# Performance work log

Measured on AMD Instinct MI355X. Metric: run time of the kernel, lower is better.

Reference implementation:

```python
import jax, jax.numpy as jnp
import numpy as np

HIDDEN = 64
EMBED = 16
N_AGENTS = 1024
TRACK_LEN = 8


def setup_inputs() -> dict:
    key = jax.random.key(0)
    ks = jax.random.split(key, 6)
    s = lambda fan_in: 1.0 / np.sqrt(fan_in)
    return {
        "hidden_state": jax.random.normal(ks[0], (1, N_AGENTS, HIDDEN), jnp.float32),
        "group_track": jax.random.normal(ks[1], (N_AGENTS, TRACK_LEN, 2), jnp.float32),
        "W_e": jax.random.normal(ks[2], (2, EMBED), jnp.float32) * s(2),
        "b_e": jnp.zeros((EMBED,), jnp.float32),
        "W1": jax.random.normal(ks[3], (EMBED + HIDDEN, 2 * HIDDEN), jnp.float32) * s(EMBED + HIDDEN),
        "b1": jnp.zeros((2 * HIDDEN,), jnp.float32),
        "W2": jax.random.normal(ks[4], (2 * HIDDEN, HIDDEN), jnp.float32) * s(2 * HIDDEN),
        "b2": jnp.zeros((HIDDEN,), jnp.float32),
    }


def reference(hidden_state, group_track, W_e, b_e, W1, b1, W2, b2):
    n = group_track.shape[0]
    ends = group_track[:, -1, :]                       # [N, 2] end positions
    # rel[c, j] = end_j - end_c  (relative neighbor end pos per center agent)
    rel = ends[None, :, :] - ends[:, None, :]          # [N, N, 2]
    emb = rel @ W_e + b_e                              # [N, N, E]
    h = jnp.broadcast_to(hidden_state[0][None, :, :], (n, n, hidden_state.shape[-1]))
    x = jnp.concatenate([h, emb], axis=-1)             # [N, N, E+H] (hidden first, as in torch)
    y = jax.nn.relu(x @ W1 + b1)                       # [N, N, 2H]
    z = jax.nn.relu(y @ W2 + b2)                       # [N, N, H]
    pooled = z.max(axis=1)                             # max over neighbors -> [N, H]
    return pooled[None]                                # [1, N, H]
```

## Files before the change

### kernel.cpp

```cpp
#include <hip/hip_runtime.h>


#define N_AG 1024

typedef __attribute__((ext_vector_type(8))) short short8;
typedef __attribute__((ext_vector_type(4))) float floatx4;
typedef __attribute__((ext_vector_type(4))) unsigned int uintx4;

#if defined(__has_builtin)
#if __has_builtin(__builtin_amdgcn_cvt_pk_bf16_f32)
#define HAVE_CVT_PK_BF16 1
typedef __bf16 bf16x2 __attribute__((ext_vector_type(2)));
#endif
#endif

__device__ __forceinline__ unsigned short f2bf(float f) {
  unsigned u = __builtin_bit_cast(unsigned, f);
  u += 0x7FFFu + ((u >> 16) & 1u);
  return (unsigned short)(u >> 16);
}

__device__ __forceinline__ unsigned pack2bf(float y0, float y1) {
#ifdef HAVE_CVT_PK_BF16
  bf16x2 pk = __builtin_amdgcn_cvt_pk_bf16_f32(y0, y1);
  return __builtin_bit_cast(unsigned, pk);
#else
  return (unsigned)f2bf(y0) | ((unsigned)f2bf(y1) << 16);
#endif
}

__global__ __launch_bounds__(128) void prep_all(
    const float* __restrict__ hidden,
    const float* __restrict__ track,
    const float* __restrict__ We,
    const float* __restrict__ be,
    const float* __restrict__ W1,
    const float* __restrict__ b1,
    const float* __restrict__ W2,
    unsigned short* __restrict__ Abf,
    float* __restrict__ M2f,
    unsigned short* __restrict__ W2T)
{
  int j = blockIdx.x;
  int k = threadIdx.x;
  __shared__ float hj[64];
  if (k < 64) hj[k] = hidden[j * 64 + k];
  __syncthreads();
  float e0 = track[j * 16 + 14];
  float e1 = track[j * 16 + 15];
  float m20 = 0.f, m21 = 0.f, cb = b1[k];
#pragma unroll
  for (int t = 0; t < 16; ++t) {
    float w1v = W1[(64 + t) * 128 + k];
    m20 += We[t] * w1v;
    m21 += We[16 + t] * w1v;
    cb  += be[t] * w1v;
  }
  float acc = e0 * m20 + e1 * m21 + cb;
#pragma unroll 16
  for (int t = 0; t < 64; ++t) acc += hj[t] * W1[t * 128 + k];
  Abf[j * 128 + k] = f2bf(acc);

  if (j == 0) {
    M2f[k]       = m20;
    M2f[128 + k] = m21;
  }
  if (j < 32) {
#pragma unroll
    for (int q = 0; q < 2; ++q) {
      int idx = j * 256 + q * 128 + k;
      int n = idx >> 7, c = idx & 127;
      W2T[n * 128 + c] = f2bf(W2[c * 64 + n]);
    }
  }
}

__global__ __launch_bounds__(256) void pool_main(
    const unsigned short* __restrict__ Abf,
    const float* __restrict__ M2f,
    const float* __restrict__ track,
    const unsigned short* __restrict__ W2T,
    const float* __restrict__ b2,
    float* __restrict__ out)
{
  const int i    = blockIdx.x;
  const int lane = threadIdx.x & 63;
  const int wave = threadIdx.x >> 6;
  const int m    = lane & 15;
  const int quad = lane >> 4;

  const float e0 = track[i * 16 + 14];
  const float e1 = track[i * 16 + 15];
  float u[4][8];
#pragma unroll
  for (int kk = 0; kk < 4; ++kk) {
#pragma unroll
    for (int jj = 0; jj < 8; ++jj) {
      int kidx = kk * 32 + quad * 8 + jj;
      u[kk][jj] = e0 * M2f[kidx] + e1 * M2f[128 + kidx];
    }
  }

  short8 bfrag[4][4];
#pragma unroll
  for (int t = 0; t < 4; ++t)
#pragma unroll
    for (int kk = 0; kk < 4; ++kk)
      bfrag[t][kk] = *(const short8*)(W2T + (t * 16 + m) * 128 + kk * 32 + quad * 8);

  floatx4 mx[4];
#pragma unroll
  for (int t = 0; t < 4; ++t) mx[t] = (floatx4){-3e38f, -3e38f, -3e38f, -3e38f};

  for (int jt = wave; jt < 64; jt += 4) {
    const unsigned short* Aptr = Abf + (jt * 16 + m) * 128 + quad * 8;
    uintx4 au[4];
#pragma unroll
    for (int kk = 0; kk < 4; ++kk) {
      uintx4 raw = *(const uintx4*)(Aptr + kk * 32);
#pragma unroll
      for (int p = 0; p < 4; ++p) {
        unsigned w = raw[p];
        float lo = __builtin_bit_cast(float, w << 16);
        float hi = __builtin_bit_cast(float, w & 0xFFFF0000u);
        float y0 = fmaxf(lo - u[kk][2 * p], 0.f);
        float y1 = fmaxf(hi - u[kk][2 * p + 1], 0.f);
        au[kk][p] = pack2bf(y0, y1);
      }
    }
#pragma unroll
    for (int t = 0; t < 4; ++t) {
      floatx4 acc = (floatx4){0.f, 0.f, 0.f, 0.f};
#pragma unroll
      for (int kk = 0; kk < 4; ++kk) {
        short8 af = __builtin_bit_cast(short8, au[kk]);
        acc = __builtin_amdgcn_mfma_f32_16x16x32_bf16(af, bfrag[t][kk], acc, 0, 0, 0);
      }
#pragma unroll
      for (int r = 0; r < 4; ++r) mx[t][r] = fmaxf(mx[t][r], acc[r]);
    }
  }

  float lm[4];
#pragma unroll
  for (int t = 0; t < 4; ++t) {
    lm[t] = fmaxf(fmaxf(mx[t][0], mx[t][1]), fmaxf(mx[t][2], mx[t][3]));
    lm[t] = fmaxf(lm[t], __shfl_xor(lm[t], 16, 64));
    lm[t] = fmaxf(lm[t], __shfl_xor(lm[t], 32, 64));
  }
  __shared__ float red[4][64];
  if (quad == 0) {
#pragma unroll
    for (int t = 0; t < 4; ++t) red[wave][t * 16 + m] = lm[t];
  }
  __syncthreads();
  if (threadIdx.x < 64) {
    int n = threadIdx.x;
    float v = fmaxf(fmaxf(red[0][n], red[1][n]), fmaxf(red[2][n], red[3][n]));
    v += b2[n];
    v = v > 0.f ? v : 0.f;
    out[i * 64 + n] = v;
  }
}

extern "C" void kernel_launch(void* const* d_in, const int* in_sizes, int n_in,
                              void* d_out, int out_size, void* d_ws, size_t ws_size,
                              hipStream_t stream) {
  const float* hidden = (const float*)d_in[0];
  const float* track  = (const float*)d_in[1];
  const float* We     = (const float*)d_in[2];
  const float* be     = (const float*)d_in[3];
  const float* W1     = (const float*)d_in[4];
  const float* b1     = (const float*)d_in[5];
  const float* W2     = (const float*)d_in[6];
  const float* b2     = (const float*)d_in[7];
  float* out = (float*)d_out;

  char* ws = (char*)d_ws;
  unsigned short* Abf = (unsigned short*)ws;
  float*          M2f = (float*)(ws + 262144);
  unsigned short* W2T = (unsigned short*)(ws + 263168);

  prep_all<<<N_AG, 128, 0, stream>>>(hidden, track, We, be, W1, b1, W2, Abf, M2f, W2T);
  pool_main<<<N_AG, 256, 0, stream>>>(Abf, M2f, track, W2T, b2, out);
}
```

Baseline: 113.5 us.

## Prefetch next A tile in pool loop and force hardware bf16 pack

The main pooling loop now issues the global loads for the next neighbor tile before the current tile's ReLU, pack and MFMA work, using register double-buffering to hide load latency. The bf16 pack now always uses inline v_cvt_pk_bf16_f32 assembly instead of the builtin-or-fallback path, so the software rounding sequence cannot be selected. The prep kernel writes the A matrix with nontemporal stores. The prefetch buffer raises register pressure, which could reduce occupancy.

```diff
diff --git a/kernel.cpp b/kernel.cpp
--- a/kernel.cpp
+++ b/kernel.cpp
@@ -7,26 +7,16 @@
 typedef __attribute__((ext_vector_type(4))) float floatx4;
 typedef __attribute__((ext_vector_type(4))) unsigned int uintx4;
 
-#if defined(__has_builtin)
-#if __has_builtin(__builtin_amdgcn_cvt_pk_bf16_f32)
-#define HAVE_CVT_PK_BF16 1
-typedef __bf16 bf16x2 __attribute__((ext_vector_type(2)));
-#endif
-#endif
-
 __device__ __forceinline__ unsigned short f2bf(float f) {
   unsigned u = __builtin_bit_cast(unsigned, f);
   u += 0x7FFFu + ((u >> 16) & 1u);
   return (unsigned short)(u >> 16);
 }
 
-__device__ __forceinline__ unsigned pack2bf(float y0, float y1) {
-#ifdef HAVE_CVT_PK_BF16
-  bf16x2 pk = __builtin_amdgcn_cvt_pk_bf16_f32(y0, y1);
-  return __builtin_bit_cast(unsigned, pk);
-#else
-  return (unsigned)f2bf(y0) | ((unsigned)f2bf(y1) << 16);
-#endif
+__device__ __forceinline__ unsigned cvtpk_bf16(float y0, float y1) {
+  unsigned r;
+  asm("v_cvt_pk_bf16_f32 %0, %1, %2" : "=v"(r) : "v"(y0), "v"(y1));
+  return r;
 }
 
 __global__ __launch_bounds__(128) void prep_all(
@@ -59,7 +49,7 @@
   float acc = e0 * m20 + e1 * m21 + cb;
 #pragma unroll 16
   for (int t = 0; t < 64; ++t) acc += hj[t] * W1[t * 128 + k];
-  Abf[j * 128 + k] = f2bf(acc);
+  __builtin_nontemporal_store(f2bf(acc), &Abf[j * 128 + k]);
 
   if (j == 0) {
     M2f[k]       = m20;
@@ -89,6 +79,11 @@
   const int m    = lane & 15;
   const int quad = lane >> 4;
 
+  const unsigned short* Aptr = Abf + (wave * 16 + m) * 128 + quad * 8;
+  uintx4 raw[4];
+#pragma unroll
+  for (int kk = 0; kk < 4; ++kk) raw[kk] = *(const uintx4*)(Aptr + kk * 32);
+
   const float e0 = track[i * 16 + 14];
   const float e1 = track[i * 16 + 15];
   float u[4][8];
@@ -113,19 +108,25 @@
   for (int t = 0; t < 4; ++t) mx[t] = (floatx4){-3e38f, -3e38f, -3e38f, -3e38f};
 
   for (int jt = wave; jt < 64; jt += 4) {
-    const unsigned short* Aptr = Abf + (jt * 16 + m) * 128 + quad * 8;
+    Aptr += 4 * 16 * 128;
+    const bool more = (jt + 4 < 64);
+    uintx4 nxt[4];
+    if (more) {
+#pragma unroll
+      for (int kk = 0; kk < 4; ++kk) nxt[kk] = *(const uintx4*)(Aptr + kk * 32);
+    }
+
     uintx4 au[4];
 #pragma unroll
     for (int kk = 0; kk < 4; ++kk) {
-      uintx4 raw = *(const uintx4*)(Aptr + kk * 32);
 #pragma unroll
       for (int p = 0; p < 4; ++p) {
-        unsigned w = raw[p];
+        unsigned w = raw[kk][p];
         float lo = __builtin_bit_cast(float, w << 16);
         float hi = __builtin_bit_cast(float, w & 0xFFFF0000u);
         float y0 = fmaxf(lo - u[kk][2 * p], 0.f);
         float y1 = fmaxf(hi - u[kk][2 * p + 1], 0.f);
-        au[kk][p] = pack2bf(y0, y1);
+        au[kk][p] = cvtpk_bf16(y0, y1);
       }
     }
 #pragma unroll
@@ -138,6 +139,10 @@
       }
 #pragma unroll
       for (int r = 0; r < 4; ++r) mx[t][r] = fmaxf(mx[t][r], acc[r]);
+    }
+    if (more) {
+#pragma unroll
+      for (int kk = 0; kk < 4; ++kk) raw[kk] = nxt[kk];
     }
   }
 
```

Result: faster. 109.8 us (-3.3%).
